# Kernel optimization log

Measured on AMD Instinct MI355X. Metric: run time of the kernel, lower is better.

The kernel has to match this reference:

```python
import jax, jax.numpy as jnp
import numpy as np

POSE, Z, H, E = 62, 32, 256, 6

def setup_inputs() -> dict:
    key = jax.random.key(0)
    ks = jax.random.split(key, 32)
    it = iter(ks)
    def W(o, i):
        return (jax.random.normal(next(it), (o, i), jnp.float32) * 0.05)
    def B(o):
        return jnp.zeros((o,), jnp.float32)
    def WE(o, i):
        return (jax.random.normal(next(it), (E, o, i), jnp.float32) * 0.05)
    def BE(o):
        return jnp.zeros((E, o), jnp.float32)
    d = {}
    d['prev_pose'] = jax.random.normal(next(it), (POSE,), jnp.float32)
    d['curr_pose'] = jax.random.normal(next(it), (POSE,), jnp.float32)
    d['eps'] = jax.random.normal(next(it), (Z,), jnp.float32)
    # encoder
    d['enc_w0'], d['enc_b0'] = W(H, POSE + POSE), B(H)
    d['enc_w1'], d['enc_b1'] = W(H, H), B(H)
    d['enc_w2'], d['enc_b2'] = W(H, H), B(H)
    d['mu_w'], d['mu_b'] = W(Z, H), B(Z)
    d['lv_w'], d['lv_b'] = W(Z, H), B(Z)
    # gating network
    d['gate_w0'], d['gate_b0'] = W(H, Z + POSE), B(H)
    d['gate_w1'], d['gate_b1'] = W(H, H), B(H)
    d['gate_w2'], d['gate_b2'] = W(H, H), B(H)
    d['gate_w3'], d['gate_b3'] = W(E, H), B(E)
    # 6 experts, stacked on leading expert axis
    d['exp_w0'], d['exp_b0'] = WE(H, Z + POSE), BE(H)
    d['exp_w1'], d['exp_b1'] = WE(H, Z + H), BE(H)
    d['exp_w2'], d['exp_b2'] = WE(H, Z + H), BE(H)
    d['exp_w3'], d['exp_b3'] = WE(POSE, Z + H), BE(POSE)
    return d

def _forward(prev_pose, curr_pose, eps,
             enc_w0, enc_b0, enc_w1, enc_b1, enc_w2, enc_b2,
             mu_w, mu_b, lv_w, lv_b,
             gate_w0, gate_b0, gate_w1, gate_b1, gate_w2, gate_b2,
             gate_w3, gate_b3,
             exp_w0, exp_b0, exp_w1, exp_b1, exp_w2, exp_b2,
             exp_w3, exp_b3):
    elu = jax.nn.elu
    # encode
    x = elu(enc_w0 @ jnp.concatenate([prev_pose, curr_pose]) + enc_b0)
    x = elu(enc_w1 @ x + enc_b1)
    x = elu(enc_w2 @ x + enc_b2)
    mu = mu_w @ x + mu_b
    logvar = lv_w @ x + lv_b
    # reparameterize (eps supplied as input for determinism)
    z = mu + eps * jnp.exp(0.5 * logvar)
    # gating network (raw logits, no softmax -- as in the original)
    g_in = jnp.concatenate([z, prev_pose])  # [94]
    g = elu(gate_w0 @ g_in + gate_b0)
    g = elu(gate_w1 @ g + gate_b1)
    g = elu(gate_w2 @ g + gate_b2)
    gates = gate_w3 @ g + gate_b3  # [6]
    # all 6 experts batched along leading axis e
    z_e = jnp.broadcast_to(z, (E, Z))  # [6,32]
    h = elu(jnp.einsum('eoh,h->eo', exp_w0, g_in) + exp_b0)       # [6,256]
    h = elu(jnp.einsum('eoh,eh->eo', exp_w1,
                       jnp.concatenate([z_e, h], axis=1)) + exp_b1)
    h = elu(jnp.einsum('eoh,eh->eo', exp_w2,
                       jnp.concatenate([z_e, h], axis=1)) + exp_b2)
    out_e = jnp.einsum('eoh,eh->eo', exp_w3,
                       jnp.concatenate([z_e, h], axis=1)) + exp_b3  # [6,62]
    decoded = jnp.sum(out_e * gates[:, None], axis=0)  # [62]
    return decoded, mu, logvar

def reference(prev_pose, curr_pose, eps,
              enc_w0, enc_b0, enc_w1, enc_b1, enc_w2, enc_b2,
              mu_w, mu_b, lv_w, lv_b,
              gate_w0, gate_b0, gate_w1, gate_b1, gate_w2, gate_b2,
              gate_w3, gate_b3,
              exp_w0, exp_b0, exp_w1, exp_b1, exp_w2, exp_b2,
              exp_w3, exp_b3):
    return _forward(prev_pose, curr_pose, eps,
                    enc_w0, enc_b0, enc_w1, enc_b1, enc_w2, enc_b2,
                    mu_w, mu_b, lv_w, lv_b,
                    gate_w0, gate_b0, gate_w1, gate_b1, gate_w2, gate_b2,
                    gate_w3, gate_b3,
                    exp_w0, exp_b0, exp_w1, exp_b1, exp_w2, exp_b2,
                    exp_w3, exp_b3)
```

## Files before the change

### kernel.cpp

```cpp
#include <hip/hip_runtime.h>
#include <math.h>


#define NWG   256
#define BLOCK 256
#define MAGIC 0x7E57A11E

__device__ __align__(128) float g_a0[256];
__device__ __align__(128) float g_a1[256];
__device__ __align__(128) float g_a2[256];
__device__ __align__(128) float g_mu[32];
__device__ __align__(128) float g_lv[32];
__device__ __align__(128) float g_g0[256];
__device__ __align__(128) float g_g1[256];
__device__ __align__(128) float g_g2[256];
__device__ __align__(128) float g_gates[32];
__device__ __align__(128) float g_h0[1536];
__device__ __align__(128) float g_h1[1536];
__device__ __align__(128) float g_h2[1536];
__device__ __align__(128) float g_oute[384];

struct P {
  const float *prev, *curr, *eps;
  const float *ew0,*eb0,*ew1,*eb1,*ew2,*eb2;
  const float *muw,*mub,*lvw,*lvb;
  const float *gw0,*gb0,*gw1,*gb1,*gw2,*gb2,*gw3,*gb3;
  const float *xw0,*xb0,*xw1,*xb1,*xw2,*xb2,*xw3,*xb3;
  float* out;
};

__device__ __forceinline__ float cload(const float* a) {
  int v = __hip_atomic_load((const int*)a, __ATOMIC_RELAXED,
                            __HIP_MEMORY_SCOPE_AGENT);
  return __int_as_float(v);
}
__device__ __forceinline__ void cstore(float* a, float v) {
  __hip_atomic_store((int*)a, __float_as_int(v), __ATOMIC_RELAXED,
                     __HIP_MEMORY_SCOPE_AGENT);
}
__device__ __forceinline__ float4 cload4(const float* a) {
  float4 r;
  r.x = cload(a + 0); r.y = cload(a + 1);
  r.z = cload(a + 2); r.w = cload(a + 3);
  return r;
}
__device__ __forceinline__ void gll16(const void* g, void* l) {
  __builtin_amdgcn_global_load_lds((const __attribute__((address_space(1))) void*)g,
                                   (__attribute__((address_space(3))) void*)l,
                                   16, 0, 0);
}
__device__ __forceinline__ void gll4(const void* g, void* l) {
  __builtin_amdgcn_global_load_lds((const __attribute__((address_space(1))) void*)g,
                                   (__attribute__((address_space(3))) void*)l,
                                   4, 0, 0);
}
__device__ __forceinline__ float wred(float v) {
#pragma unroll
  for (int m = 32; m; m >>= 1) v += __shfl_xor(v, m, 64);
  return v;
}
__device__ __forceinline__ float elu(float x) { return x > 0.f ? x : expm1f(x); }
__device__ __forceinline__ float dot4(float4 a, float4 b) {
  return a.x*b.x + a.y*b.y + a.z*b.z + a.w*b.w;
}

__device__ __forceinline__ int* slotp(int* flags, int ph, int wg) {
  return &flags[((ph - 1) * NWG + wg) * 16];
}
__device__ __forceinline__ void bar_arrive(int* flags, int ph) {
  __syncthreads();
  if (threadIdx.x == 0)
    __hip_atomic_store(slotp(flags, ph, blockIdx.x), MAGIC,
                       __ATOMIC_RELAXED, __HIP_MEMORY_SCOPE_AGENT);
}
__device__ __forceinline__ void bar_poll(int* flags, int ph) {
  if (threadIdx.x < 64) {
    const int l = threadIdx.x;
    for (;;) {
      int v0 = __hip_atomic_load(slotp(flags, ph, l),       __ATOMIC_RELAXED, __HIP_MEMORY_SCOPE_AGENT);
      int v1 = __hip_atomic_load(slotp(flags, ph, l +  64), __ATOMIC_RELAXED, __HIP_MEMORY_SCOPE_AGENT);
      int v2 = __hip_atomic_load(slotp(flags, ph, l + 128), __ATOMIC_RELAXED, __HIP_MEMORY_SCOPE_AGENT);
      int v3 = __hip_atomic_load(slotp(flags, ph, l + 192), __ATOMIC_RELAXED, __HIP_MEMORY_SCOPE_AGENT);
      if (v0 == MAGIC && v1 == MAGIC && v2 == MAGIC && v3 == MAGIC) break;
      __builtin_amdgcn_s_sleep(2);
    }
  }
  __syncthreads();
}
__device__ __forceinline__ void gridbar(int* flags, int ph) {
  bar_arrive(flags, ph);
  bar_poll(flags, ph);
}

__global__ __launch_bounds__(BLOCK, 1) void mvae_main(P p, int* flags) {
  const int tid  = threadIdx.x;
  const int lane = tid & 63;
  const int wvin = tid >> 6;
  const int Wv   = blockIdx.x * 4 + wvin;

  __shared__ __align__(16) float s_w1[4][256];
  __shared__ __align__(16) float s_w2[4][256];
  __shared__ __align__(16) float s_w3[4][256];
  __shared__ __align__(16) float s_w4[4][2][96];
  __shared__ __align__(16) float s_w5[4][2][288];
  __shared__ __align__(16) float s_w6[4][2][288];
  __shared__ __align__(16) float s_w7[4][288];
  __shared__ float s_o[384];
  __shared__ float s_gg[8];

  if (Wv < 256) {
    gll16(p.ew1 + Wv * 256 + lane * 4, s_w1[wvin]);
    gll16(p.ew2 + Wv * 256 + lane * 4, s_w2[wvin]);
  }
  if (Wv < 64) {
    const float* src = (Wv < 32) ? p.muw + Wv * 256 : p.lvw + (Wv - 32) * 256;
    gll16(src + lane * 4, s_w3[wvin]);
  }
#pragma unroll
  for (int k = 0; k < 2; ++k) {
    int r = Wv + 1024 * k;
    if (r < 1792) {
      const float* src = (r < 256) ? p.gw0 + r * 94 : p.xw0 + (size_t)(r - 256) * 94;
      float* dst = s_w4[wvin][k];
      if (lane < 23)       gll16(src + lane * 4, dst);
      else if (lane == 23) { gll4(src + 92, dst + 69);
                             gll4(src + 93, dst + 70); }
    }
  }
#pragma unroll
  for (int k = 0; k < 2; ++k) {
    int r = Wv + 1024 * k;
    if (r < 1792) {
      float* dst = s_w5[wvin][k];
      if (r < 256) gll16(p.gw1 + r * 256 + lane * 4, dst);
      else {
        const float* src = p.xw1 + (size_t)(r - 256) * 288;
        gll16(src + lane * 4, dst);
        if (lane < 8) gll16(src + 256 + lane * 4, dst + 256);
      }
    }
  }
#pragma unroll
  for (int k = 0; k < 2; ++k) {
    int r = Wv + 1024 * k;
    if (r < 1792) {
      float* dst = s_w6[wvin][k];
      if (r < 256) gll16(p.gw2 + r * 256 + lane * 4, dst);
      else {
        const float* src = p.xw2 + (size_t)(r - 256) * 288;
        gll16(src + lane * 4, dst);
        if (lane < 8) gll16(src + 256 + lane * 4, dst + 256);
      }
    }
  }
  if (Wv < 6) {
    gll16(p.gw3 + Wv * 256 + lane * 4, s_w7[wvin]);
  } else if (Wv < 378) {
    const float* src = p.xw3 + (size_t)(Wv - 6) * 288;
    float* dst = s_w7[wvin];
    gll16(src + lane * 4, dst);
    if (lane < 8) gll16(src + 256 + lane * 4, dst + 256);
  }

  if (Wv < 256) {
    const float* wr = p.ew0 + Wv * 124;
    float wa = wr[lane];
    float wb = (lane < 60) ? wr[64 + lane] : 0.f;
    float xa = (lane < 62) ? p.prev[lane] : p.curr[lane - 62];
    float xb = (lane < 60) ? p.curr[lane + 2] : 0.f;
    float s = wred(wa * xa + wb * xb);
    if (!lane) cstore(&g_a0[Wv], elu(s + p.eb0[Wv]));
  }
  gridbar(flags, 1);

  if (Wv < 256) {
    float4 w = *(const float4*)(s_w1[wvin] + 4 * lane);
    float4 x = cload4(g_a0 + 4 * lane);
    float s = wred(dot4(w, x));
    if (!lane) cstore(&g_a1[Wv], elu(s + p.eb1[Wv]));
  }
  gridbar(flags, 2);

  if (Wv < 256) {
    float4 w = *(const float4*)(s_w2[wvin] + 4 * lane);
    float4 x = cload4(g_a1 + 4 * lane);
    float s = wred(dot4(w, x));
    if (!lane) cstore(&g_a2[Wv], elu(s + p.eb2[Wv]));
  }
  gridbar(flags, 3);

  if (Wv < 64) {
    float4 w = *(const float4*)(s_w3[wvin] + 4 * lane);
    float4 x = cload4(g_a2 + 4 * lane);
    float s = wred(dot4(w, x));
    if (!lane) {
      if (Wv < 32) { float v = s + p.mub[Wv]; cstore(&g_mu[Wv], v); p.out[62 + Wv] = v; }
      else { int r = Wv - 32; float v = s + p.lvb[r]; cstore(&g_lv[r], v); p.out[94 + r] = v; }
    }
  }
  gridbar(flags, 4);

  float zs = 0.f;
  if (lane < 32)
    zs = cload(&g_mu[lane]) + p.eps[lane] * expf(0.5f * cload(&g_lv[lane]));
  float4 z4;
  z4.x = __shfl(zs, (4 * lane + 0) & 63, 64);
  z4.y = __shfl(zs, (4 * lane + 1) & 63, 64);
  z4.z = __shfl(zs, (4 * lane + 2) & 63, 64);
  z4.w = __shfl(zs, (4 * lane + 3) & 63, 64);
  float prevA = (lane >= 32 && lane < 94) ? p.prev[lane - 32] : 0.f;
  float prevB = (lane < 30) ? p.prev[32 + lane] : 0.f;
  float xa94 = (lane < 32) ? zs : prevA;

#pragma unroll
  for (int k = 0; k < 2; ++k) {
    int r = Wv + 1024 * k;
    if (r < 1792) {
      const float* wrow = s_w4[wvin][k];
      float wa = wrow[lane];
      float wb = (lane < 30) ? wrow[64 + lane] : 0.f;
      float s = wred(wa * xa94 + wb * prevB);
      if (!lane) {
        if (r < 256) cstore(&g_g0[r], elu(s + p.gb0[r]));
        else         cstore(&g_h0[r - 256], elu(s + p.xb0[r - 256]));
      }
    }
  }
  gridbar(flags, 5);

#pragma unroll
  for (int k = 0; k < 2; ++k) {
    int r = Wv + 1024 * k;
    if (r < 1792) {
      const float* wrow = s_w5[wvin][k];
      float4 w = *(const float4*)(wrow + 4 * lane);
      if (r < 256) {
        float4 x = cload4(g_g0 + 4 * lane);
        float s = wred(dot4(w, x));
        if (!lane) cstore(&g_g1[r], elu(s + p.gb1[r]));
      } else {
        int q = r - 256, e = q >> 8;
        const float* hsrc = g_h0 + e * 256;
        float4 xh = z4;
        if (lane >= 8) xh = cload4(hsrc + 4 * lane - 32);
        float s = dot4(w, xh);
        if (lane < 32) s += wrow[256 + lane] * cload(hsrc + 224 + lane);
        s = wred(s);
        if (!lane) cstore(&g_h1[q], elu(s + p.xb1[q]));
      }
    }
  }
  gridbar(flags, 6);

#pragma unroll
  for (int k = 0; k < 2; ++k) {
    int r = Wv + 1024 * k;
    if (r < 1792) {
      const float* wrow = s_w6[wvin][k];
      float4 w = *(const float4*)(wrow + 4 * lane);
      if (r < 256) {
        float4 x = cload4(g_g1 + 4 * lane);
        float s = wred(dot4(w, x));
        if (!lane) cstore(&g_g2[r], elu(s + p.gb2[r]));
      } else {
        int q = r - 256, e = q >> 8;
        const float* hsrc = g_h1 + e * 256;
        float4 xh = z4;
        if (lane >= 8) xh = cload4(hsrc + 4 * lane - 32);
        float s = dot4(w, xh);
        if (lane < 32) s += wrow[256 + lane] * cload(hsrc + 224 + lane);
        s = wred(s);
        if (!lane) cstore(&g_h2[q], elu(s + p.xb2[q]));
      }
    }
  }
  gridbar(flags, 7);

  if (Wv < 6) {
    float4 w = *(const float4*)(s_w7[wvin] + 4 * lane);
    float4 x = cload4(g_g2 + 4 * lane);
    float s = wred(dot4(w, x));
    if (!lane) cstore(&g_gates[Wv], s + p.gb3[Wv]);
  } else if (Wv < 378) {
    int q = Wv - 6, e = q / 62;
    const float* wrow = s_w7[wvin];
    float4 w = *(const float4*)(wrow + 4 * lane);
    const float* hsrc = g_h2 + e * 256;
    float4 xh = z4;
    if (lane >= 8) xh = cload4(hsrc + 4 * lane - 32);
    float s = dot4(w, xh);
    if (lane < 32) s += wrow[256 + lane] * cload(hsrc + 224 + lane);
    s = wred(s);
    if (!lane) cstore(&g_oute[q], s + p.xb3[q]);
  }

  bar_arrive(flags, 8);
  if (blockIdx.x != 0) return;
  bar_poll(flags, 8);

  s_o[tid] = cload(&g_oute[tid]);
  if (tid < 116) s_o[tid + 256] = cload(&g_oute[tid + 256]);
  if (tid < 6)   s_gg[tid] = cload(&g_gates[tid]);
  __syncthreads();
  if (tid < 62) {
    float s = 0.f;
#pragma unroll
    for (int e = 0; e < 6; ++e) s += s_o[e * 62 + tid] * s_gg[e];
    p.out[tid] = s;
  }

#pragma unroll
  for (int ph = 1; ph <= 8; ++ph)
    __hip_atomic_store(slotp(flags, ph, tid), 0,
                       __ATOMIC_RELAXED, __HIP_MEMORY_SCOPE_AGENT);
}

extern "C" void kernel_launch(void* const* d_in, const int* in_sizes, int n_in,
                              void* d_out, int out_size, void* d_ws, size_t ws_size,
                              hipStream_t stream) {
  (void)in_sizes; (void)n_in; (void)out_size; (void)ws_size;
  const float* const* in = (const float* const*)d_in;
  P p;
  p.prev = in[0];  p.curr = in[1];  p.eps = in[2];
  p.ew0 = in[3];   p.eb0 = in[4];   p.ew1 = in[5];  p.eb1 = in[6];
  p.ew2 = in[7];   p.eb2 = in[8];
  p.muw = in[9];   p.mub = in[10];  p.lvw = in[11]; p.lvb = in[12];
  p.gw0 = in[13];  p.gb0 = in[14];  p.gw1 = in[15]; p.gb1 = in[16];
  p.gw2 = in[17];  p.gb2 = in[18];  p.gw3 = in[19]; p.gb3 = in[20];
  p.xw0 = in[21];  p.xb0 = in[22];  p.xw1 = in[23]; p.xb1 = in[24];
  p.xw2 = in[25];  p.xb2 = in[26];  p.xw3 = in[27]; p.xb3 = in[28];
  p.out = (float*)d_out;

  int* flags = (int*)d_ws;
  mvae_main<<<NWG, BLOCK, 0, stream>>>(p, flags);
}
```

Baseline: 32.66 us.

## Halve workgroups, split grid barriers, and overlap weight prefetch with barrier waits

Cuts the persistent grid from 256 to 128 workgroups, each wave now handling up to four rows per layer. The grid barrier is split into arrive and poll, and the shared-memory weight prefetches for later layers are issued between them so loads overlap the wait. Polls only check the workgroups that produced data for the phase (64 or 16 instead of all). This shortens the upfront load burst and lowers barrier polling cost, but doubles per-wave serial work in the expert layers and raises LDS use per workgroup.

```diff
diff --git a/kernel.cpp b/kernel.cpp
--- a/kernel.cpp
+++ b/kernel.cpp
@@ -2,9 +2,10 @@
 #include <math.h>
 
 
-#define NWG   256
-#define BLOCK 256
-#define MAGIC 0x7E57A11E
+#define NWG    128
+#define NWAVES (NWG * 4)
+#define BLOCK  256
+#define MAGIC  0x7E57A11E
 
 __device__ __align__(128) float g_a0[256];
 __device__ __align__(128) float g_a1[256];
@@ -73,23 +74,20 @@
     __hip_atomic_store(slotp(flags, ph, blockIdx.x), MAGIC,
                        __ATOMIC_RELAXED, __HIP_MEMORY_SCOPE_AGENT);
 }
-__device__ __forceinline__ void bar_poll(int* flags, int ph) {
+__device__ __forceinline__ void bar_poll(int* flags, int ph, int nprod) {
   if (threadIdx.x < 64) {
     const int l = threadIdx.x;
     for (;;) {
-      int v0 = __hip_atomic_load(slotp(flags, ph, l),       __ATOMIC_RELAXED, __HIP_MEMORY_SCOPE_AGENT);
-      int v1 = __hip_atomic_load(slotp(flags, ph, l +  64), __ATOMIC_RELAXED, __HIP_MEMORY_SCOPE_AGENT);
-      int v2 = __hip_atomic_load(slotp(flags, ph, l + 128), __ATOMIC_RELAXED, __HIP_MEMORY_SCOPE_AGENT);
-      int v3 = __hip_atomic_load(slotp(flags, ph, l + 192), __ATOMIC_RELAXED, __HIP_MEMORY_SCOPE_AGENT);
-      if (v0 == MAGIC && v1 == MAGIC && v2 == MAGIC && v3 == MAGIC) break;
+      bool ok = true;
+      for (int w = l; w < nprod; w += 64)
+        ok &= (__hip_atomic_load(slotp(flags, ph, w),
+                                 __ATOMIC_RELAXED, __HIP_MEMORY_SCOPE_AGENT)
+               == MAGIC);
+      if (ok) break;
       __builtin_amdgcn_s_sleep(2);
     }
   }
   __syncthreads();
-}
-__device__ __forceinline__ void gridbar(int* flags, int ph) {
-  bar_arrive(flags, ph);
-  bar_poll(flags, ph);
 }
 
 __global__ __launch_bounds__(BLOCK, 1) void mvae_main(P p, int* flags) {
@@ -101,66 +99,15 @@
   __shared__ __align__(16) float s_w1[4][256];
   __shared__ __align__(16) float s_w2[4][256];
   __shared__ __align__(16) float s_w3[4][256];
-  __shared__ __align__(16) float s_w4[4][2][96];
-  __shared__ __align__(16) float s_w5[4][2][288];
-  __shared__ __align__(16) float s_w6[4][2][288];
+  __shared__ __align__(16) float s_w4[4][4][96];
+  __shared__ __align__(16) float s_w5[4][4][288];
+  __shared__ __align__(16) float s_w6[4][4][288];
   __shared__ __align__(16) float s_w7[4][288];
   __shared__ float s_o[384];
   __shared__ float s_gg[8];
 
-  if (Wv < 256) {
+  if (Wv < 256)
     gll16(p.ew1 + Wv * 256 + lane * 4, s_w1[wvin]);
-    gll16(p.ew2 + Wv * 256 + lane * 4, s_w2[wvin]);
-  }
-  if (Wv < 64) {
-    const float* src = (Wv < 32) ? p.muw + Wv * 256 : p.lvw + (Wv - 32) * 256;
-    gll16(src + lane * 4, s_w3[wvin]);
-  }
-#pragma unroll
-  for (int k = 0; k < 2; ++k) {
-    int r = Wv + 1024 * k;
-    if (r < 1792) {
-      const float* src = (r < 256) ? p.gw0 + r * 94 : p.xw0 + (size_t)(r - 256) * 94;
-      float* dst = s_w4[wvin][k];
-      if (lane < 23)       gll16(src + lane * 4, dst);
-      else if (lane == 23) { gll4(src + 92, dst + 69);
-                             gll4(src + 93, dst + 70); }
-    }
-  }
-#pragma unroll
-  for (int k = 0; k < 2; ++k) {
-    int r = Wv + 1024 * k;
-    if (r < 1792) {
-      float* dst = s_w5[wvin][k];
-      if (r < 256) gll16(p.gw1 + r * 256 + lane * 4, dst);
-      else {
-        const float* src = p.xw1 + (size_t)(r - 256) * 288;
-        gll16(src + lane * 4, dst);
-        if (lane < 8) gll16(src + 256 + lane * 4, dst + 256);
-      }
-    }
-  }
-#pragma unroll
-  for (int k = 0; k < 2; ++k) {
-    int r = Wv + 1024 * k;
-    if (r < 1792) {
-      float* dst = s_w6[wvin][k];
-      if (r < 256) gll16(p.gw2 + r * 256 + lane * 4, dst);
-      else {
-        const float* src = p.xw2 + (size_t)(r - 256) * 288;
-        gll16(src + lane * 4, dst);
-        if (lane < 8) gll16(src + 256 + lane * 4, dst + 256);
-      }
-    }
-  }
-  if (Wv < 6) {
-    gll16(p.gw3 + Wv * 256 + lane * 4, s_w7[wvin]);
-  } else if (Wv < 378) {
-    const float* src = p.xw3 + (size_t)(Wv - 6) * 288;
-    float* dst = s_w7[wvin];
-    gll16(src + lane * 4, dst);
-    if (lane < 8) gll16(src + 256 + lane * 4, dst + 256);
-  }
 
   if (Wv < 256) {
     const float* wr = p.ew0 + Wv * 124;
@@ -171,7 +118,14 @@
     float s = wred(wa * xa + wb * xb);
     if (!lane) cstore(&g_a0[Wv], elu(s + p.eb0[Wv]));
   }
-  gridbar(flags, 1);
+  bar_arrive(flags, 1);
+  if (Wv < 256)
+    gll16(p.ew2 + Wv * 256 + lane * 4, s_w2[wvin]);
+  if (Wv < 64) {
+    const float* src = (Wv < 32) ? p.muw + Wv * 256 : p.lvw + (Wv - 32) * 256;
+    gll16(src + lane * 4, s_w3[wvin]);
+  }
+  bar_poll(flags, 1, 64);
 
   if (Wv < 256) {
     float4 w = *(const float4*)(s_w1[wvin] + 4 * lane);
@@ -179,7 +133,32 @@
     float s = wred(dot4(w, x));
     if (!lane) cstore(&g_a1[Wv], elu(s + p.eb1[Wv]));
   }
-  gridbar(flags, 2);
+  bar_arrive(flags, 2);
+#pragma unroll
+  for (int k = 0; k < 4; ++k) {
+    int r = Wv + NWAVES * k;
+    if (r < 1792) {
+      const float* src = (r < 256) ? p.gw0 + r * 94 : p.xw0 + (size_t)(r - 256) * 94;
+      float* dst = s_w4[wvin][k];
+      if (lane < 23)       gll16(src + lane * 4, dst);
+      else if (lane == 23) { gll4(src + 92, dst + 69);
+                             gll4(src + 93, dst + 70); }
+    }
+  }
+#pragma unroll
+  for (int k = 0; k < 4; ++k) {
+    int r = Wv + NWAVES * k;
+    if (r < 1792) {
+      float* dst = s_w5[wvin][k];
+      if (r < 256) gll16(p.gw1 + r * 256 + lane * 4, dst);
+      else {
+        const float* src = p.xw1 + (size_t)(r - 256) * 288;
+        gll16(src + lane * 4, dst);
+        if (lane < 8) gll16(src + 256 + lane * 4, dst + 256);
+      }
+    }
+  }
+  bar_poll(flags, 2, 64);
 
   if (Wv < 256) {
     float4 w = *(const float4*)(s_w2[wvin] + 4 * lane);
@@ -187,7 +166,29 @@
     float s = wred(dot4(w, x));
     if (!lane) cstore(&g_a2[Wv], elu(s + p.eb2[Wv]));
   }
-  gridbar(flags, 3);
+  bar_arrive(flags, 3);
+#pragma unroll
+  for (int k = 0; k < 4; ++k) {
+    int r = Wv + NWAVES * k;
+    if (r < 1792) {
+      float* dst = s_w6[wvin][k];
+      if (r < 256) gll16(p.gw2 + r * 256 + lane * 4, dst);
+      else {
+        const float* src = p.xw2 + (size_t)(r - 256) * 288;
+        gll16(src + lane * 4, dst);
+        if (lane < 8) gll16(src + 256 + lane * 4, dst + 256);
+      }
+    }
+  }
+  if (Wv < 6) {
+    gll16(p.gw3 + Wv * 256 + lane * 4, s_w7[wvin]);
+  } else if (Wv < 378) {
+    const float* src = p.xw3 + (size_t)(Wv - 6) * 288;
+    float* dst = s_w7[wvin];
+    gll16(src + lane * 4, dst);
+    if (lane < 8) gll16(src + 256 + lane * 4, dst + 256);
+  }
+  bar_poll(flags, 3, 64);
 
   if (Wv < 64) {
     float4 w = *(const float4*)(s_w3[wvin] + 4 * lane);
@@ -198,7 +199,8 @@
       else { int r = Wv - 32; float v = s + p.lvb[r]; cstore(&g_lv[r], v); p.out[94 + r] = v; }
     }
   }
-  gridbar(flags, 4);
+  bar_arrive(flags, 4);
+  bar_poll(flags, 4, 16);
 
   float zs = 0.f;
   if (lane < 32)
@@ -213,8 +215,8 @@
   float xa94 = (lane < 32) ? zs : prevA;
 
 #pragma unroll
-  for (int k = 0; k < 2; ++k) {
-    int r = Wv + 1024 * k;
+  for (int k = 0; k < 4; ++k) {
+    int r = Wv + NWAVES * k;
     if (r < 1792) {
       const float* wrow = s_w4[wvin][k];
       float wa = wrow[lane];
@@ -226,11 +228,12 @@
       }
     }
   }
-  gridbar(flags, 5);
-
-#pragma unroll
-  for (int k = 0; k < 2; ++k) {
-    int r = Wv + 1024 * k;
+  bar_arrive(flags, 5);
+  bar_poll(flags, 5, NWG);
+
+#pragma unroll
+  for (int k = 0; k < 4; ++k) {
+    int r = Wv + NWAVES * k;
     if (r < 1792) {
       const float* wrow = s_w5[wvin][k];
       float4 w = *(const float4*)(wrow + 4 * lane);
@@ -250,11 +253,12 @@
       }
     }
   }
-  gridbar(flags, 6);
-
-#pragma unroll
-  for (int k = 0; k < 2; ++k) {
-    int r = Wv + 1024 * k;
+  bar_arrive(flags, 6);
+  bar_poll(flags, 6, NWG);
+
+#pragma unroll
+  for (int k = 0; k < 4; ++k) {
+    int r = Wv + NWAVES * k;
     if (r < 1792) {
       const float* wrow = s_w6[wvin][k];
       float4 w = *(const float4*)(wrow + 4 * lane);
@@ -274,7 +278,8 @@
       }
     }
   }
-  gridbar(flags, 7);
+  bar_arrive(flags, 7);
+  bar_poll(flags, 7, NWG);
 
   if (Wv < 6) {
     float4 w = *(const float4*)(s_w7[wvin] + 4 * lane);
@@ -296,7 +301,7 @@
 
   bar_arrive(flags, 8);
   if (blockIdx.x != 0) return;
-  bar_poll(flags, 8);
+  bar_poll(flags, 8, NWG);
 
   s_o[tid] = cload(&g_oute[tid]);
   if (tid < 116) s_o[tid + 256] = cload(&g_oute[tid + 256]);
@@ -309,9 +314,8 @@
     p.out[tid] = s;
   }
 
-#pragma unroll
-  for (int ph = 1; ph <= 8; ++ph)
-    __hip_atomic_store(slotp(flags, ph, tid), 0,
+  for (int idx = tid; idx < 8 * NWG; idx += BLOCK)
+    __hip_atomic_store(&flags[idx * 16], 0,
                        __ATOMIC_RELAXED, __HIP_MEMORY_SCOPE_AGENT);
 }
 
```

Measured after the change: 33.08 us. About the same (+1.3%).
